# Kernel optimization log

Hardware: AMD Instinct MI355X
Metric: run time of the kernel (lower is better)

Reference implementation:

```python
import jax, jax.numpy as jnp
import numpy as np

IMG = 128   # source volume edge
OUT = 64    # resized crop edge
MIN_CROP = 15


def setup_inputs() -> dict:
    key = jax.random.key(0)
    k1, k2, k3 = jax.random.split(key, 3)
    B, N = 4, 64
    x = jax.random.normal(k1, (B, 1, IMG, IMG, IMG), dtype=jnp.float32)
    # crop_size = max(15, int(rand()*128)), matching the torch module
    sizes = jnp.maximum((jax.random.uniform(k2, (B, N)) * IMG).astype(jnp.int32), MIN_CROP)
    # start uniform in [0, IMG - size]
    u = jax.random.uniform(k3, (B, N, 3))
    starts = jnp.floor(u * (IMG - sizes[..., None]).astype(jnp.float32)).astype(jnp.int32)
    return {"x": x, "crop_sizes": sizes, "crop_starts": starts}


def _axis_coords(start, size):
    # torch trilinear interpolate, align_corners=False: src = (dst+0.5)*scale - 0.5
    j = jnp.arange(OUT, dtype=jnp.float32)
    sz = size.astype(jnp.float32)
    src = (j + 0.5) * (sz / OUT) - 0.5
    src = jnp.clip(src, 0.0, sz - 1.0)
    i0 = jnp.floor(src).astype(jnp.int32)
    i1 = jnp.minimum(i0 + 1, size - 1)
    w = src - i0.astype(jnp.float32)
    return start + i0, start + i1, w


def _crop_resize(vol, start, size):
    # vol: [IMG,IMG,IMG]; start: [3] int; size: scalar int -> [OUT,OUT,OUT]
    d0, d1, wd = _axis_coords(start[0], size)
    h0, h1, wh = _axis_coords(start[1], size)
    w0, w1, ww = _axis_coords(start[2], size)

    def g(a, b, c):
        return vol[a[:, None, None], b[None, :, None], c[None, None, :]]

    wd = wd[:, None, None]
    wh = wh[None, :, None]
    ww = ww[None, None, :]
    c00 = g(d0, h0, w0) * (1 - ww) + g(d0, h0, w1) * ww
    c01 = g(d0, h1, w0) * (1 - ww) + g(d0, h1, w1) * ww
    c10 = g(d1, h0, w0) * (1 - ww) + g(d1, h0, w1) * ww
    c11 = g(d1, h1, w0) * (1 - ww) + g(d1, h1, w1) * ww
    c0 = c00 * (1 - wh) + c01 * wh
    c1 = c10 * (1 - wh) + c11 * wh
    return c0 * (1 - wd) + c1 * wd


def reference(x, crop_sizes, crop_starts):
    vols = x[:, 0]  # [B,IMG,IMG,IMG]
    per_crop = jax.vmap(_crop_resize, in_axes=(None, 0, 0))
    per_batch = jax.vmap(per_crop, in_axes=(0, 0, 0))
    out = per_batch(vols, crop_starts, crop_sizes)  # [B,N,OUT,OUT,OUT]
    B, N = out.shape[0], out.shape[1]
    return out.reshape(B * N, 1, OUT, OUT, OUT)
```

## Files before the change

kernel.cpp:

```cpp
#include <hip/hip_runtime.h>

#define IMG 128
#define PLANE (IMG * IMG)
#define VOLSZ (IMG * IMG * IMG)

typedef float f4a __attribute__((ext_vector_type(4), aligned(4)));
typedef float f2a __attribute__((ext_vector_type(2), aligned(8)));

__global__ __launch_bounds__(256) void crop_resize_kernel(
    const float* __restrict__ x,
    const int* __restrict__ sizes,
    const int* __restrict__ starts,
    float* __restrict__ out)
{
    int bid  = blockIdx.x;
    int swz  = (bid & 7) * 2048 + (bid >> 3);
    int crop = swz >> 6;
    int d_o  = swz & 63;
    int b    = crop >> 6;

    int sz  = sizes[crop];
    int s_d = starts[crop * 3 + 0];
    int s_h = starts[crop * 3 + 1];
    int s_w = starts[crop * 3 + 2];

    float szf   = (float)sz;
    float scale = szf * (1.0f / 64.0f);
    float szm1  = szf - 1.0f;
    int   szm2  = sz - 2;

    int lane = threadIdx.x & 63;
    int wid  = __builtin_amdgcn_readfirstlane((int)threadIdx.x >> 6);
    int wp   = lane & 31;
    int hsel = lane >> 5;

    auto axis = [&](int j, int& i0, float& fr) {
        float src = ((float)j + 0.5f) * scale - 0.5f;
        src = fminf(fmaxf(src, 0.0f), szm1);
        i0 = min((int)src, szm2);
        fr = src - (float)i0;
    };

    int ih; float fh;
    axis(lane, ih, fh);
    int ho0 = (s_h + ih) * IMG;

    int i00, i01; float fw0, fw1;
    axis(2 * wp,     i00, fw0);
    axis(2 * wp + 1, i01, fw1);
    float omw0 = 1.0f - fw0, omw1 = 1.0f - fw1;

    int anc   = min(s_w + i00, IMG - 4);
    int sig   = s_w + i00 - anc;
    int sigd  = sig + (i01 - i00);
    bool a1 = (sig  >= 1), a2 = (sig  >= 2);
    bool b1 = (sigd >= 1), b2 = (sigd >= 2);

    int id; float wd_;
    axis(d_o, id, wd_);
    float wd = wd_;

    const float* prow = x + (long long)b * VOLSZ + (s_d + id) * PLANE + anc;

    float* oblk = out + ((long long)crop * 64 + d_o) * 4096 + 2 * wp;

    #pragma unroll
    for (int it = 0; it < 8; ++it) {
        int hA = it * 8 + wid * 2;
        int rA = __builtin_amdgcn_readlane(ho0, hA);
        int rB = __builtin_amdgcn_readlane(ho0, hA + 1);
        float wA = __int_as_float(__builtin_amdgcn_readlane(__float_as_int(fh), hA));
        float wB = __int_as_float(__builtin_amdgcn_readlane(__float_as_int(fh), hA + 1));

        int   rh = hsel ? rB : rA;
        float wh = hsel ? wB : wA;

        const float* r00 = prow + rh;
        f4a va = *(const f4a*)(r00);
        f4a vb = *(const f4a*)(r00 + IMG);
        f4a vc = *(const f4a*)(r00 + PLANE);
        f4a vd = *(const f4a*)(r00 + PLANE + IMG);

        auto wl = [&](f4a v, float& o0, float& o1) {
            float p0 = a1 ? (a2 ? v.z : v.y) : v.x;
            float p1 = a1 ? (a2 ? v.w : v.z) : v.y;
            float q0 = b1 ? (b2 ? v.z : v.y) : v.x;
            float q1 = b1 ? (b2 ? v.w : v.z) : v.y;
            o0 = p0 * omw0 + p1 * fw0;
            o1 = q0 * omw1 + q1 * fw1;
        };
        float a0, a1v, b0, b1v, c0, c1v, d0, d1v;
        wl(va, a0, a1v);
        wl(vb, b0, b1v);
        wl(vc, c0, c1v);
        wl(vd, d0, d1v);

        float e00 = a0  + (b0  - a0)  * wh;
        float e01 = a1v + (b1v - a1v) * wh;
        float e10 = c0  + (d0  - c0)  * wh;
        float e11 = c1v + (d1v - c1v) * wh;

        f2a res;
        res.x = e00 + (e10 - e00) * wd;
        res.y = e01 + (e11 - e01) * wd;

        __builtin_nontemporal_store(res, (f2a*)(oblk + (hA + hsel) * 64));
    }
}

extern "C" void kernel_launch(void* const* d_in, const int* in_sizes, int n_in,
                              void* d_out, int out_size, void* d_ws, size_t ws_size,
                              hipStream_t stream) {
    const float* x      = (const float*)d_in[0];
    const int*   sizes  = (const int*)d_in[1];
    const int*   starts = (const int*)d_in[2];
    float*       out    = (float*)d_out;

    int blocks = 256 * 64;
    crop_resize_kernel<<<blocks, 256, 0, stream>>>(x, sizes, starts, out);
}
```

Baseline: 110.8 us.

## Reorder crops by depth start so concurrent blocks share cached source planes

Adds a small ranking kernel that sorts each batch's 64 crops by their depth start coordinate and writes a permutation into the workspace. The main kernel then maps block slots to crops through this permutation, so crops processed around the same time read overlapping depth slabs of the source volume and reuse L2/MALL lines. This costs an extra kernel launch and a dependent perm lookup per block, and output order is unchanged because the crop index is only used for addressing.

```diff
diff --git a/kernel.cpp b/kernel.cpp
--- a/kernel.cpp
+++ b/kernel.cpp
@@ -7,17 +7,38 @@
 typedef float f4a __attribute__((ext_vector_type(4), aligned(4)));
 typedef float f2a __attribute__((ext_vector_type(2), aligned(8)));
 
+__global__ __launch_bounds__(256) void rank_kernel(
+    const int* __restrict__ starts, int* __restrict__ perm)
+{
+    __shared__ int keys[256];
+    int t = threadIdx.x;
+    int v = t >> 6;
+    int j = t & 63;
+    int sd = starts[t * 3];
+    keys[t] = (sd << 6) | j;
+    __syncthreads();
+    int key = keys[t];
+    int rank = 0;
+    #pragma unroll
+    for (int k = 0; k < 64; ++k)
+        rank += (keys[(v << 6) + k] < key) ? 1 : 0;
+    perm[(v << 6) + rank] = j;
+}
+
 __global__ __launch_bounds__(256) void crop_resize_kernel(
     const float* __restrict__ x,
     const int* __restrict__ sizes,
     const int* __restrict__ starts,
+    const int* __restrict__ perm,
     float* __restrict__ out)
 {
     int bid  = blockIdx.x;
     int swz  = (bid & 7) * 2048 + (bid >> 3);
-    int crop = swz >> 6;
+    int v    = swz >> 12;
+    int slot = (swz >> 6) & 63;
     int d_o  = swz & 63;
-    int b    = crop >> 6;
+    int crop = (v << 6) + perm[(v << 6) + slot];
+    int b    = v;
 
     int sz  = sizes[crop];
     int s_d = starts[crop * 3 + 0];
@@ -81,11 +102,11 @@
         f4a vc = *(const f4a*)(r00 + PLANE);
         f4a vd = *(const f4a*)(r00 + PLANE + IMG);
 
-        auto wl = [&](f4a v, float& o0, float& o1) {
-            float p0 = a1 ? (a2 ? v.z : v.y) : v.x;
-            float p1 = a1 ? (a2 ? v.w : v.z) : v.y;
-            float q0 = b1 ? (b2 ? v.z : v.y) : v.x;
-            float q1 = b1 ? (b2 ? v.w : v.z) : v.y;
+        auto wl = [&](f4a vv, float& o0, float& o1) {
+            float p0 = a1 ? (a2 ? vv.z : vv.y) : vv.x;
+            float p1 = a1 ? (a2 ? vv.w : vv.z) : vv.y;
+            float q0 = b1 ? (b2 ? vv.z : vv.y) : vv.x;
+            float q1 = b1 ? (b2 ? vv.w : vv.z) : vv.y;
             o0 = p0 * omw0 + p1 * fw0;
             o1 = q0 * omw1 + q1 * fw1;
         };
@@ -115,7 +136,10 @@
     const int*   sizes  = (const int*)d_in[1];
     const int*   starts = (const int*)d_in[2];
     float*       out    = (float*)d_out;
+    int*         perm   = (int*)d_ws;
+
+    rank_kernel<<<1, 256, 0, stream>>>(starts, perm);
 
     int blocks = 256 * 64;
-    crop_resize_kernel<<<blocks, 256, 0, stream>>>(x, sizes, starts, out);
+    crop_resize_kernel<<<blocks, 256, 0, stream>>>(x, sizes, starts, perm, out);
 }
```

Measured after the change: 121.3 us. 9.5% more time.

## Compute two output depth slices per block, sharing source planes

Applied to the files above, without the earlier changes.

Each block now produces two adjacent output depth slices instead of one, and the grid is halved. Before loading, it checks how far apart the two slices' source depth indices are. If they are equal or adjacent, the source planes they share are loaded and interpolated once, which cuts redundant global loads and H/W interpolation work. The cost is three branch variants (more code, more registers) and half as many blocks, which lowers parallelism on a kernel that is mostly bound by the output stores.

```diff
diff --git a/kernel.cpp b/kernel.cpp
--- a/kernel.cpp
+++ b/kernel.cpp
@@ -14,9 +14,9 @@
     float* __restrict__ out)
 {
     int bid  = blockIdx.x;
-    int swz  = (bid & 7) * 2048 + (bid >> 3);
-    int crop = swz >> 6;
-    int d_o  = swz & 63;
+    int swz  = (bid & 7) * 1024 + (bid >> 3);
+    int crop = swz >> 5;
+    int k    = swz & 31;
     int b    = crop >> 6;
 
     int sz  = sizes[crop];
@@ -53,59 +53,93 @@
     int anc   = min(s_w + i00, IMG - 4);
     int sig   = s_w + i00 - anc;
     int sigd  = sig + (i01 - i00);
-    bool a1 = (sig  >= 1), a2 = (sig  >= 2);
-    bool b1 = (sigd >= 1), b2 = (sigd >= 2);
+    bool s1 = (sig  >= 1), s2 = (sig  >= 2);
+    bool t1 = (sigd >= 1), t2 = (sigd >= 2);
 
-    int id; float wd_;
-    axis(d_o, id, wd_);
-    float wd = wd_;
+    int id0, id1; float wd0, wd1;
+    axis(2 * k,     id0, wd0);
+    axis(2 * k + 1, id1, wd1);
+    int dd = id1 - id0;
 
-    const float* prow = x + (long long)b * VOLSZ + (s_d + id) * PLANE + anc;
+    const float* prow = x + (long long)b * VOLSZ + (s_d + id0) * PLANE + anc;
 
-    float* oblk = out + ((long long)crop * 64 + d_o) * 4096 + 2 * wp;
+    float* orow0 = out + ((long long)crop * 64 + 2 * k) * 4096 + 2 * wp;
+    float* orow1 = orow0 + 4096;
 
-    #pragma unroll
-    for (int it = 0; it < 8; ++it) {
-        int hA = it * 8 + wid * 2;
-        int rA = __builtin_amdgcn_readlane(ho0, hA);
-        int rB = __builtin_amdgcn_readlane(ho0, hA + 1);
-        float wA = __int_as_float(__builtin_amdgcn_readlane(__float_as_int(fh), hA));
-        float wB = __int_as_float(__builtin_amdgcn_readlane(__float_as_int(fh), hA + 1));
+    auto wl = [&](f4a v, float& o0, float& o1) {
+        float p0 = s1 ? (s2 ? v.z : v.y) : v.x;
+        float p1 = s1 ? (s2 ? v.w : v.z) : v.y;
+        float q0 = t1 ? (t2 ? v.z : v.y) : v.x;
+        float q1 = t1 ? (t2 ? v.w : v.z) : v.y;
+        o0 = p0 * omw0 + p1 * fw0;
+        o1 = q0 * omw1 + q1 * fw1;
+    };
+    auto planeU = [&](const float* r, int qo, float wh_, float& u0, float& u1) {
+        f4a lo = *(const f4a*)(r + qo);
+        f4a hi = *(const f4a*)(r + qo + IMG);
+        float l0, l1, h0v, h1v;
+        wl(lo, l0, l1);
+        wl(hi, h0v, h1v);
+        u0 = l0 + (h0v - l0) * wh_;
+        u1 = l1 + (h1v - l1) * wh_;
+    };
 
-        int   rh = hsel ? rB : rA;
-        float wh = hsel ? wB : wA;
+    #define ITER_HEAD                                                        \
+        int hA = it * 8 + wid * 2;                                           \
+        int rA = __builtin_amdgcn_readlane(ho0, hA);                         \
+        int rB = __builtin_amdgcn_readlane(ho0, hA + 1);                     \
+        float wA = __int_as_float(__builtin_amdgcn_readlane(__float_as_int(fh), hA));      \
+        float wB = __int_as_float(__builtin_amdgcn_readlane(__float_as_int(fh), hA + 1));  \
+        int   rh = hsel ? rB : rA;                                           \
+        float wh = hsel ? wB : wA;                                           \
+        const float* r = prow + rh;                                          \
+        int so = (hA + hsel) * 64;
 
-        const float* r00 = prow + rh;
-        f4a va = *(const f4a*)(r00);
-        f4a vb = *(const f4a*)(r00 + IMG);
-        f4a vc = *(const f4a*)(r00 + PLANE);
-        f4a vd = *(const f4a*)(r00 + PLANE + IMG);
-
-        auto wl = [&](f4a v, float& o0, float& o1) {
-            float p0 = a1 ? (a2 ? v.z : v.y) : v.x;
-            float p1 = a1 ? (a2 ? v.w : v.z) : v.y;
-            float q0 = b1 ? (b2 ? v.z : v.y) : v.x;
-            float q1 = b1 ? (b2 ? v.w : v.z) : v.y;
-            o0 = p0 * omw0 + p1 * fw0;
-            o1 = q0 * omw1 + q1 * fw1;
-        };
-        float a0, a1v, b0, b1v, c0, c1v, d0, d1v;
-        wl(va, a0, a1v);
-        wl(vb, b0, b1v);
-        wl(vc, c0, c1v);
-        wl(vd, d0, d1v);
-
-        float e00 = a0  + (b0  - a0)  * wh;
-        float e01 = a1v + (b1v - a1v) * wh;
-        float e10 = c0  + (d0  - c0)  * wh;
-        float e11 = c1v + (d1v - c1v) * wh;
-
-        f2a res;
-        res.x = e00 + (e10 - e00) * wd;
-        res.y = e01 + (e11 - e01) * wd;
-
-        __builtin_nontemporal_store(res, (f2a*)(oblk + (hA + hsel) * 64));
+    if (dd == 0) {
+        #pragma unroll
+        for (int it = 0; it < 8; ++it) {
+            ITER_HEAD
+            float u00, u01, u10, u11;
+            planeU(r, 0,     wh, u00, u01);
+            planeU(r, PLANE, wh, u10, u11);
+            f2a r0, r1;
+            r0.x = u00 + (u10 - u00) * wd0;  r0.y = u01 + (u11 - u01) * wd0;
+            r1.x = u00 + (u10 - u00) * wd1;  r1.y = u01 + (u11 - u01) * wd1;
+            __builtin_nontemporal_store(r0, (f2a*)(orow0 + so));
+            __builtin_nontemporal_store(r1, (f2a*)(orow1 + so));
+        }
+    } else if (dd == 1) {
+        #pragma unroll
+        for (int it = 0; it < 8; ++it) {
+            ITER_HEAD
+            float u00, u01, u10, u11, u20, u21;
+            planeU(r, 0,         wh, u00, u01);
+            planeU(r, PLANE,     wh, u10, u11);
+            planeU(r, 2 * PLANE, wh, u20, u21);
+            f2a r0, r1;
+            r0.x = u00 + (u10 - u00) * wd0;  r0.y = u01 + (u11 - u01) * wd0;
+            r1.x = u10 + (u20 - u10) * wd1;  r1.y = u11 + (u21 - u11) * wd1;
+            __builtin_nontemporal_store(r0, (f2a*)(orow0 + so));
+            __builtin_nontemporal_store(r1, (f2a*)(orow1 + so));
+        }
+    } else {
+        int o2 = dd * PLANE, o3 = o2 + PLANE;
+        #pragma unroll
+        for (int it = 0; it < 8; ++it) {
+            ITER_HEAD
+            float u00, u01, u10, u11, u20, u21, u30, u31;
+            planeU(r, 0,     wh, u00, u01);
+            planeU(r, PLANE, wh, u10, u11);
+            planeU(r, o2,    wh, u20, u21);
+            planeU(r, o3,    wh, u30, u31);
+            f2a r0, r1;
+            r0.x = u00 + (u10 - u00) * wd0;  r0.y = u01 + (u11 - u01) * wd0;
+            r1.x = u20 + (u30 - u20) * wd1;  r1.y = u21 + (u31 - u21) * wd1;
+            __builtin_nontemporal_store(r0, (f2a*)(orow0 + so));
+            __builtin_nontemporal_store(r1, (f2a*)(orow1 + so));
+        }
     }
+    #undef ITER_HEAD
 }
 
 extern "C" void kernel_launch(void* const* d_in, const int* in_sizes, int n_in,
@@ -116,6 +150,6 @@
     const int*   starts = (const int*)d_in[2];
     float*       out    = (float*)d_out;
 
-    int blocks = 256 * 64;
+    int blocks = 256 * 32;
     crop_resize_kernel<<<blocks, 256, 0, stream>>>(x, sizes, starts, out);
 }
```

New measurement: 101.1 us. -8.8%, faster.

## Stream source depth planes per block and reuse width-height interpolants across output depths

Applied to the files above, without the earlier changes.

Each block now covers 16 output depth slices for 8 output rows instead of one depth slice for all 64 rows. It walks the source depth planes in order and keeps the previous plane's width-height interpolated values in registers, so each source plane is loaded once and shared by every output depth that falls between two planes. The aim is to cut redundant global loads, since neighbouring output depths sample the same source planes when crops are small. In exchange the block runs a data-dependent serial loop with ballot and readlane work per plane, and has fewer blocks overall, which may cost parallelism when crops are large.

```diff
diff --git a/kernel.cpp b/kernel.cpp
--- a/kernel.cpp
+++ b/kernel.cpp
@@ -14,9 +14,11 @@
     float* __restrict__ out)
 {
     int bid  = blockIdx.x;
-    int swz  = (bid & 7) * 2048 + (bid >> 3);
-    int crop = swz >> 6;
-    int d_o  = swz & 63;
+    int swz  = (bid & 7) * 1024 + (bid >> 3);
+    int crop = swz >> 5;
+    int rem  = swz & 31;
+    int hsl8 = (rem >> 2) << 3;
+    int dq16 = (rem & 3) << 4;
     int b    = crop >> 6;
 
     int sz  = sizes[crop];
@@ -32,7 +34,7 @@
     int lane = threadIdx.x & 63;
     int wid  = __builtin_amdgcn_readfirstlane((int)threadIdx.x >> 6);
     int wp   = lane & 31;
-    int hsel = lane >> 5;
+    int hs   = lane >> 5;
 
     auto axis = [&](int j, int& i0, float& fr) {
         float src = ((float)j + 0.5f) * scale - 0.5f;
@@ -41,70 +43,74 @@
         fr = src - (float)i0;
     };
 
-    int ih; float fh;
-    axis(lane, ih, fh);
-    int ho0 = (s_h + ih) * IMG;
-
     int i00, i01; float fw0, fw1;
     axis(2 * wp,     i00, fw0);
     axis(2 * wp + 1, i01, fw1);
     float omw0 = 1.0f - fw0, omw1 = 1.0f - fw1;
 
-    int anc   = min(s_w + i00, IMG - 4);
-    int sig   = s_w + i00 - anc;
-    int sigd  = sig + (i01 - i00);
-    bool a1 = (sig  >= 1), a2 = (sig  >= 2);
-    bool b1 = (sigd >= 1), b2 = (sigd >= 2);
+    int anc  = min(s_w + i00, IMG - 4);
+    int sig  = s_w + i00 - anc;
+    int sigd = sig + (i01 - i00);
+    bool s1 = (sig  >= 1), s2 = (sig  >= 2);
+    bool t1 = (sigd >= 1), t2 = (sigd >= 2);
 
-    int id; float wd_;
-    axis(d_o, id, wd_);
-    float wd = wd_;
+    int hrow = hsl8 + wid * 2 + hs;
+    int ihh; float fh;
+    axis(hrow, ihh, fh);
 
-    const float* prow = x + (long long)b * VOLSZ + (s_d + id) * PLANE + anc;
+    int idj; float fdj;
+    axis(dq16 + (lane & 15), idj, fdj);
 
-    float* oblk = out + ((long long)crop * 64 + d_o) * 4096 + 2 * wp;
+    int p0   = __builtin_amdgcn_readlane(idj, 0);
+    int pend = __builtin_amdgcn_readlane(idj, 15) + 1;
 
-    #pragma unroll
-    for (int it = 0; it < 8; ++it) {
-        int hA = it * 8 + wid * 2;
-        int rA = __builtin_amdgcn_readlane(ho0, hA);
-        int rB = __builtin_amdgcn_readlane(ho0, hA + 1);
-        float wA = __int_as_float(__builtin_amdgcn_readlane(__float_as_int(fh), hA));
-        float wB = __int_as_float(__builtin_amdgcn_readlane(__float_as_int(fh), hA + 1));
+    const float* sp = x + (long long)b * VOLSZ
+                    + (s_d + p0) * PLANE + (s_h + ihh) * IMG + anc;
 
-        int   rh = hsel ? rB : rA;
-        float wh = hsel ? wB : wA;
+    float* ob = out + ((long long)crop * 64) * 4096 + hrow * 64 + 2 * wp;
 
-        const float* r00 = prow + rh;
-        f4a va = *(const f4a*)(r00);
-        f4a vb = *(const f4a*)(r00 + IMG);
-        f4a vc = *(const f4a*)(r00 + PLANE);
-        f4a vd = *(const f4a*)(r00 + PLANE + IMG);
+    auto wl = [&](f4a v, float& o0, float& o1) {
+        float p0v = s1 ? (s2 ? v.z : v.y) : v.x;
+        float p1v = s1 ? (s2 ? v.w : v.z) : v.y;
+        float q0v = t1 ? (t2 ? v.z : v.y) : v.x;
+        float q1v = t1 ? (t2 ? v.w : v.z) : v.y;
+        o0 = p0v * omw0 + p1v * fw0;
+        o1 = q0v * omw1 + q1v * fw1;
+    };
 
-        auto wl = [&](f4a v, float& o0, float& o1) {
-            float p0 = a1 ? (a2 ? v.z : v.y) : v.x;
-            float p1 = a1 ? (a2 ? v.w : v.z) : v.y;
-            float q0 = b1 ? (b2 ? v.z : v.y) : v.x;
-            float q1 = b1 ? (b2 ? v.w : v.z) : v.y;
-            o0 = p0 * omw0 + p1 * fw0;
-            o1 = q0 * omw1 + q1 * fw1;
-        };
-        float a0, a1v, b0, b1v, c0, c1v, d0, d1v;
-        wl(va, a0, a1v);
-        wl(vb, b0, b1v);
-        wl(vc, c0, c1v);
-        wl(vd, d0, d1v);
+    f4a rlo = *(const f4a*)(sp);
+    f4a rhi = *(const f4a*)(sp + IMG);
 
-        float e00 = a0  + (b0  - a0)  * wh;
-        float e01 = a1v + (b1v - a1v) * wh;
-        float e10 = c0  + (d0  - c0)  * wh;
-        float e11 = c1v + (d1v - c1v) * wh;
+    float a0 = 0.0f, a1 = 0.0f;
 
-        f2a res;
-        res.x = e00 + (e10 - e00) * wd;
-        res.y = e01 + (e11 - e01) * wd;
+    for (int p = p0; p <= pend; ++p) {
+        const float* spn = sp + (p < pend ? PLANE : 0);
+        f4a nlo = *(const f4a*)(spn);
+        f4a nhi = *(const f4a*)(spn + IMG);
 
-        __builtin_nontemporal_store(res, (f2a*)(oblk + (hA + hsel) * 64));
+        float l0, l1, g0, g1;
+        wl(rlo, l0, l1);
+        wl(rhi, g0, g1);
+        float b0v = l0 + (g0 - l0) * fh;
+        float b1v = l1 + (g1 - l1) * fh;
+
+        if (p > p0) {
+            unsigned long long m = __ballot(idj == (p - 1)) & 0xFFFFull;
+            while (m) {
+                int dr = __ffsll((unsigned long long)m) - 1;
+                m &= m - 1;
+                float wd = __int_as_float(
+                    __builtin_amdgcn_readlane(__float_as_int(fdj), dr));
+                f2a r;
+                r.x = a0 + (b0v - a0) * wd;
+                r.y = a1 + (b1v - a1) * wd;
+                __builtin_nontemporal_store(r,
+                    (f2a*)(ob + (long long)(dq16 + dr) * 4096));
+            }
+        }
+        a0 = b0v; a1 = b1v;
+        rlo = nlo; rhi = nhi;
+        sp  = spn;
     }
 }
 
@@ -116,6 +122,6 @@
     const int*   starts = (const int*)d_in[2];
     float*       out    = (float*)d_out;
 
-    int blocks = 256 * 64;
+    int blocks = 256 * 32;
     crop_resize_kernel<<<blocks, 256, 0, stream>>>(x, sizes, starts, out);
 }
```

Result: faster. 90.60 us (-18.2%).
